# Kernel tuning notes

Hardware: AMD Instinct MI355X
Metric: run time of the kernel (lower is better)

The kernel has to match this reference:

```python
import jax, jax.numpy as jnp
import numpy as np

B, C, H, W = 4, 128, 96, 96
INTER = C // 2


def setup_inputs() -> dict:
    key = jax.random.key(0)
    ks = jax.random.split(key, 6)
    scale = 1.0 / np.sqrt(C)
    return {
        "x1": jax.random.normal(ks[0], (B, C, H, W), dtype=jnp.float32),
        "x2": jax.random.normal(ks[1], (B, C, H, W), dtype=jnp.float32),
        "w_theta": jax.random.normal(ks[2], (INTER, C), dtype=jnp.float32) * scale,
        "w_phi": jax.random.normal(ks[3], (INTER, C), dtype=jnp.float32) * scale,
        "w_g": jax.random.normal(ks[4], (INTER, C), dtype=jnp.float32) * scale,
        "w_mask": jax.random.normal(ks[5], (C, INTER), dtype=jnp.float32) * (1.0 / np.sqrt(INTER)),
    }


def reference(x1, x2, w_theta, w_phi, w_g, w_mask):
    b, c, h1, w1 = x1.shape  # c == full channel
    inter = c // 2
    # 1x1 convs (no bias) == channel GEMMs
    theta = jnp.einsum('ic,bchw->bihw', w_theta, x1)   # [b, inter, h1, w1]
    phi   = jnp.einsum('ic,bchw->bihw', w_phi,   x2)   # [b, inter, h2, w2]
    g     = jnp.einsum('ic,bchw->bihw', w_g,     x2)   # [b, inter, h2, w2]
    # Faithful to original: .view(b, c, -1) with c = FULL channel count,
    # so the flattened length is H*W/2 and the contraction dim is c (row-major reshape).
    theta = theta.reshape(b, c, -1).transpose(0, 2, 1)  # [b, N1, c], N1 = h1*w1//2
    phi = phi.reshape(b, c, -1)                         # [b, c, N2]
    g = g.reshape(b, c, -1).transpose(0, 2, 1)          # [b, N2, c]
    scores = jnp.einsum('bnc,bcm->bnm', theta, phi)     # [b, N1, N2]
    attn = jax.nn.softmax(scores, axis=1)               # softmax over dim=1 (query axis!)
    y = jnp.einsum('bnm,bmc->bnc', attn, g)             # [b, N1, c]
    y = y.transpose(0, 2, 1).reshape(b, inter, h1, w1)  # [b, inter, h1, w1]
    mask = jnp.einsum('ci,bihw->bchw', w_mask, y)       # [b, c, h1, w1]
    return mask + x1
```

## Files before the change

### kernel.cpp

```cpp
#include <hip/hip_runtime.h>

typedef __attribute__((ext_vector_type(8))) short short8;
typedef __attribute__((ext_vector_type(4))) float f32x4;
typedef __attribute__((ext_vector_type(16))) float f32x16;
typedef unsigned short u16;
typedef unsigned int u32;

#define NB 4
#define CH 128
#define INTER2 64
#define HW2 9216
#define NN 4608
#define NSLICE 8
#define SLW 576
#define SK 8
#define PCH 136

__device__ __forceinline__ u16 f2bf(float f) {
  u32 u = __float_as_uint(f);
  u += 0x7fffu + ((u >> 16) & 1u);
  return (u16)(u >> 16);
}
__device__ __forceinline__ float bf2f(u16 h) { return __uint_as_float(((u32)h) << 16); }
__device__ __forceinline__ u32 cvtpk(float lo, float hi) {
  u32 r;
  asm("v_cvt_pk_bf16_f32 %0, %1, %2" : "=v"(r) : "v"(lo), "v"(hi));
  return r;
}
__device__ __forceinline__ void gl_lds16(const u16* g, u16* l) {
  __builtin_amdgcn_global_load_lds(
      (const __attribute__((address_space(1))) unsigned int*)g,
      (__attribute__((address_space(3))) unsigned int*)l, 16, 0, 0);
}

__global__ void k_wcvt(const float* __restrict__ wt, const float* __restrict__ wp,
                       const float* __restrict__ wg, const float* __restrict__ wm,
                       u16* __restrict__ wtb, u16* __restrict__ wpb,
                       u16* __restrict__ wgb, u16* __restrict__ wmb) {
  int i = blockIdx.x * 256 + threadIdx.x;
  if (i < CH * INTER2) {
    wtb[i] = f2bf(wt[i]);
    wpb[i] = f2bf(wp[i]);
    wgb[i] = f2bf(wg[i]);
    wmb[i] = f2bf(wm[i]);
  }
}

__global__ __launch_bounds__(256) void k_conv(const float* __restrict__ x1,
                                              const float* __restrict__ x2,
                                              const u16* __restrict__ wtb,
                                              const u16* __restrict__ wpb,
                                              const u16* __restrict__ wgb,
                                              u16* __restrict__ Tt,
                                              u16* __restrict__ Pt,
                                              u16* __restrict__ Gn) {
  __shared__ u16 xT[64 * PCH];
  __shared__ u16 ot[64 * 72];
  const int tid = threadIdx.x;
  const int w = tid >> 6, l = tid & 63, lr = l & 15, lg = l >> 4;
  const int pt = blockIdx.x, b = blockIdx.y, z = blockIdx.z;
  const int p0 = pt * 64;
  const int h = (p0 >= NN) ? 1 : 0;
  const int n0 = p0 - h * NN;
  const float* X = (z ? x2 : x1) + (size_t)b * CH * HW2;

  {
    const int pq = (l & 15) * 4;
    const int cs = w + 4 * (l >> 4);
#pragma unroll
    for (int it = 0; it < 8; it++) {
      const int c = it * 16 + cs;
      float4 v = *(const float4*)(X + (size_t)c * HW2 + p0 + pq);
      xT[(pq + 0) * PCH + c] = f2bf(v.x);
      xT[(pq + 1) * PCH + c] = f2bf(v.y);
      xT[(pq + 2) * PCH + c] = f2bf(v.z);
      xT[(pq + 3) * PCH + c] = f2bf(v.w);
    }
  }
  short8 wsP[4], wsG[4];
  {
    const u16* W1 = z ? wpb : wtb;
#pragma unroll
    for (int ks = 0; ks < 4; ks++)
      wsP[ks] = *(const short8*)(W1 + (w * 16 + lr) * CH + ks * 32 + lg * 8);
    if (z) {
#pragma unroll
      for (int ks = 0; ks < 4; ks++)
        wsG[ks] = *(const short8*)(wgb + (w * 16 + lr) * CH + ks * 32 + lg * 8);
    }
  }
  __syncthreads();
  short8 xf[4][4];
#pragma unroll
  for (int tp = 0; tp < 4; tp++)
#pragma unroll
    for (int ks = 0; ks < 4; ks++)
      xf[tp][ks] = *(const short8*)(&xT[(tp * 16 + lr) * PCH + ks * 32 + lg * 8]);

  f32x4 accP[4];
#pragma unroll
  for (int tp = 0; tp < 4; tp++) {
#pragma unroll
    for (int j = 0; j < 4; j++) accP[tp][j] = 0.f;
#pragma unroll
    for (int ks = 0; ks < 4; ks++)
      accP[tp] = __builtin_amdgcn_mfma_f32_16x16x32_bf16(xf[tp][ks], wsP[ks], accP[tp], 0, 0, 0);
  }
#pragma unroll
  for (int tp = 0; tp < 4; tp++) {
#pragma unroll
    for (int j = 0; j < 4; j++)
      ot[(tp * 16 + lg * 4 + j) * 72 + w * 16 + lr] = f2bf(accP[tp][j]);
  }
  if (z) {
    f32x4 accG[4];
#pragma unroll
    for (int tp = 0; tp < 4; tp++) {
#pragma unroll
      for (int j = 0; j < 4; j++) accG[tp][j] = 0.f;
#pragma unroll
      for (int ks = 0; ks < 4; ks++)
        accG[tp] = __builtin_amdgcn_mfma_f32_16x16x32_bf16(wsG[ks], xf[tp][ks], accG[tp], 0, 0, 0);
    }
    u16* Gb = Gn + (size_t)b * CH * NN;
#pragma unroll
    for (int tp = 0; tp < 4; tp++) {
#pragma unroll
      for (int j = 0; j < 4; j++) {
        const int ig = w * 16 + lg * 4 + j;
        Gb[(size_t)((h << 6) + ig) * NN + n0 + tp * 16 + lr] = f2bf(accG[tp][j]);
      }
    }
  }
  __syncthreads();
  {
    u16* dst = (z ? Pt : Tt) + (size_t)b * NN * CH;
#pragma unroll
    for (int q = 0; q < 2; q++) {
      const int idx = tid * 2 + q;
      const int p = idx >> 3, c8 = (idx & 7) * 8;
      uint4 v = *(const uint4*)(&ot[p * 72 + c8]);
      *(uint4*)(dst + (size_t)(n0 + p) * CH + h * 64 + c8) = v;
    }
  }
}

__global__ __launch_bounds__(256) void k_scores(const u16* __restrict__ Tt,
                                                const u16* __restrict__ Pt,
                                                u16* __restrict__ E,
                                                float* __restrict__ denp,
                                                int b0) {
  __shared__ u16 Et[64 * 72];
  const int tid = threadIdx.x;
  const int w = tid >> 6, l = tid & 63, lm = l & 31, lh = l >> 5;
  const int wm2 = w >> 1, wn2 = w & 1;
  const int s = blockIdx.x & 7, mt = blockIdx.x >> 3;
  const int eb = blockIdx.y, b = b0 + eb;
  const int m0 = mt * 64;
  const int nbase = s * SLW;
  const u16* PtB = Pt + (size_t)b * NN * CH;
  const u16* TtB = Tt + (size_t)b * NN * CH;
  u16* Eb = E + (size_t)eb * NN * NN;

  short8 bf[8];
#pragma unroll
  for (int ks = 0; ks < 8; ks++)
    bf[ks] = *(const short8*)(PtB + (size_t)(m0 + wm2 * 32 + lm) * CH + ks * 16 + lh * 8);

  float den_l = 0.f;
  short8 ac[8], an[8];
#pragma unroll
  for (int ks = 0; ks < 8; ks++)
    ac[ks] = *(const short8*)(TtB + (size_t)(nbase + wn2 * 32 + lm) * CH + ks * 16 + lh * 8);

  for (int it = 0; it < 9; it++) {
    if (it + 1 < 9) {
      const int nr = nbase + (it + 1) * 64 + wn2 * 32 + lm;
#pragma unroll
      for (int ks = 0; ks < 8; ks++)
        an[ks] = *(const short8*)(TtB + (size_t)nr * CH + ks * 16 + lh * 8);
    }
    f32x16 acc;
#pragma unroll
    for (int q = 0; q < 16; q++) acc[q] = 0.f;
#pragma unroll
    for (int ks = 0; ks < 8; ks++)
      acc = __builtin_amdgcn_mfma_f32_32x32x16_bf16(ac[ks], bf[ks], acc, 0, 0, 0);
#pragma unroll
    for (int q = 0; q < 16; q += 2) {
      const int nl = wn2 * 32 + (q & 3) + 8 * (q >> 2) + 4 * lh;
      float e0 = exp2f(__builtin_fmaf(acc[q], 1.44269504f, -57.70780163f));
      float e1 = exp2f(__builtin_fmaf(acc[q + 1], 1.44269504f, -57.70780163f));
      den_l += e0;
      den_l += e1;
      u32 pk = cvtpk(e0, e1);
      Et[nl * 72 + wm2 * 32 + lm] = (u16)pk;
      Et[(nl + 1) * 72 + wm2 * 32 + lm] = (u16)(pk >> 16);
    }
    __syncthreads();
    {
      const int row0 = tid >> 3, col = (tid & 7) * 8;
      const int ng = nbase + it * 64;
#pragma unroll
      for (int p = 0; p < 2; p++) {
        const int r2 = p * 32 + row0;
        uint4 v = *(const uint4*)(&Et[r2 * 72 + col]);
        *(uint4*)(Eb + (size_t)(ng + r2) * NN + m0 + col) = v;
      }
    }
    __syncthreads();
    if (it + 1 < 9) {
#pragma unroll
      for (int ks = 0; ks < 8; ks++) ac[ks] = an[ks];
    }
  }
  den_l += __shfl_xor(den_l, 32, 64);
  __shared__ float dl[4][32];
  if (l < 32) dl[w][l] = den_l;
  __syncthreads();
  if (tid < 64)
    denp[(size_t)(s * NB + b) * NN + m0 + tid] =
        dl[(tid >> 5) * 2][tid & 31] + dl[(tid >> 5) * 2 + 1][tid & 31];
}

__global__ __launch_bounds__(256) void k_gd(const u16* __restrict__ Gn,
                                            const float* __restrict__ denp,
                                            u16* __restrict__ Gd,
                                            int b0) {
  const int q = blockIdx.x * 256 + threadIdx.x;
  const int d = q / 576, mc = q % 576;
  const int m0 = mc * 8;
  const int b = b0 + blockIdx.y;
  float dn[8];
#pragma unroll
  for (int i = 0; i < 8; i++) dn[i] = 0.f;
#pragma unroll
  for (int s = 0; s < NSLICE; s++) {
    const float* dp = denp + (size_t)(s * NB + b) * NN + m0;
    float4 a = *(const float4*)dp;
    float4 c = *(const float4*)(dp + 4);
    dn[0] += a.x; dn[1] += a.y; dn[2] += a.z; dn[3] += a.w;
    dn[4] += c.x; dn[5] += c.y; dn[6] += c.z; dn[7] += c.w;
  }
  const size_t off = (size_t)b * CH * NN + (size_t)d * NN + m0;
  uint4 v = *(const uint4*)(Gn + off);
  u32 arr[4] = {v.x, v.y, v.z, v.w};
  uint4 o;
  u32 ov[4];
#pragma unroll
  for (int j = 0; j < 4; j++) {
    float lo = bf2f((u16)(arr[j] & 0xffffu)) / dn[2 * j];
    float hi = bf2f((u16)(arr[j] >> 16)) / dn[2 * j + 1];
    ov[j] = cvtpk(lo, hi);
  }
  o.x = ov[0]; o.y = ov[1]; o.z = ov[2]; o.w = ov[3];
  *(uint4*)(Gd + off) = o;
}

__global__ __launch_bounds__(256) void k_pv(const u16* __restrict__ E,
                                            const u16* __restrict__ Gd,
                                            float* __restrict__ Yp,
                                            int b0) {
  __shared__ u16 lA[128 * 64];
  __shared__ u16 lB[128 * 64];
  const int tid = threadIdx.x;
  const int w = tid >> 6, l = tid & 63, lr = l & 15, lg = l >> 4;
  const int sk = blockIdx.x / 36, nt = blockIdx.x % 36;
  const int eb = blockIdx.y, b = b0 + eb;
  const int n0 = nt * 128;
  const int k0 = sk * (NN / SK);
  const u16* Eb = E + (size_t)eb * NN * NN;
  const u16* Gb = Gd + (size_t)b * CH * NN;
  const int wm = w >> 1, wn2 = w & 1;
  const int rl = l >> 3;
  const int cg = (l & 7) ^ rl;

  f32x4 acc[4][4];
#pragma unroll
  for (int fa = 0; fa < 4; fa++)
#pragma unroll
    for (int fb = 0; fb < 4; fb++)
#pragma unroll
      for (int j = 0; j < 4; j++) acc[fa][fb][j] = 0.f;

#define STAGE(kk)                                                                   \
  {                                                                                 \
    _Pragma("unroll") for (int r = 0; r < 4; r++) {                                 \
      const int rowA = r * 32 + w * 8 + rl;                                         \
      gl_lds16(Gb + (size_t)rowA * NN + (kk) + cg * 8, &lA[(r * 32 + w * 8) * 64]); \
      gl_lds16(Eb + (size_t)(n0 + rowA) * NN + (kk) + cg * 8,                       \
               &lB[(r * 32 + w * 8) * 64]);                                         \
    }                                                                               \
  }

  STAGE(k0);
  const int NKS = (NN / SK) / 64;
  for (int st = 0; st < NKS; st++) {
    __syncthreads();
#pragma unroll
    for (int ks2 = 0; ks2 < 2; ks2++) {
      const int cw = ((ks2 * 4 + lg) ^ (lr & 7)) * 8;
      short8 af[4], bfr[4];
#pragma unroll
      for (int fa = 0; fa < 4; fa++)
        af[fa] = *(const short8*)(&lA[(wm * 64 + fa * 16 + lr) * 64 + cw]);
#pragma unroll
      for (int fb = 0; fb < 4; fb++)
        bfr[fb] = *(const short8*)(&lB[(wn2 * 64 + fb * 16 + lr) * 64 + cw]);
#pragma unroll
      for (int fa = 0; fa < 4; fa++)
#pragma unroll
        for (int fb = 0; fb < 4; fb++)
          acc[fa][fb] = __builtin_amdgcn_mfma_f32_16x16x32_bf16(af[fa], bfr[fb], acc[fa][fb], 0, 0, 0);
    }
    __syncthreads();
    if (st + 1 < NKS) STAGE(k0 + (st + 1) * 64);
  }
#undef STAGE
  const int slab = sk * 2 + eb;
  float* Yb = Yp + (size_t)slab * CH * NN;
#pragma unroll
  for (int fa = 0; fa < 4; fa++) {
#pragma unroll
    for (int fb = 0; fb < 4; fb++) {
      const int n = n0 + wn2 * 64 + fb * 16 + lr;
#pragma unroll
      for (int j = 0; j < 4; j++) {
        const int cc = wm * 64 + fa * 16 + lg * 4 + j;
        Yb[(size_t)cc * NN + n] = acc[fa][fb][j];
      }
    }
  }
}

__global__ __launch_bounds__(256) void k_out(const float* __restrict__ Yp,
                                             const u16* __restrict__ wmb,
                                             const float* __restrict__ x1,
                                             float* __restrict__ out,
                                             int b0) {
  __shared__ u16 yy[64][72];
  const int tid = threadIdx.x;
  const int w = tid >> 6, l = tid & 63, lr = l & 15, lg = l >> 4;
  const int eb = blockIdx.y, b = b0 + eb;
  const int n0 = blockIdx.x * 32;
  const int nl = tid & 31, cch = tid >> 5;

  float v[16];
#pragma unroll
  for (int q = 0; q < 16; q++) v[q] = 0.f;
  for (int s2 = 0; s2 < SK; s2++) {
    const float* base = Yp + ((size_t)(s2 * 2 + eb) * CH + cch * 16) * NN + n0 + nl;
#pragma unroll
    for (int q = 0; q < 16; q++) v[q] += base[(size_t)q * NN];
  }
#pragma unroll
  for (int q = 0; q < 16; q++) {
    const int d = cch * 16 + q;
    yy[(d >> 6) * 32 + nl][d & 63] = f2bf(v[q]);
  }
  __syncthreads();

  const int wm3 = w >> 1, wp3 = w & 1;
  f32x4 eacc[4][2];
#pragma unroll
  for (int fa = 0; fa < 4; fa++)
#pragma unroll
    for (int fb = 0; fb < 2; fb++)
#pragma unroll
      for (int j = 0; j < 4; j++) eacc[fa][fb][j] = 0.f;
#pragma unroll
  for (int ks = 0; ks < 2; ks++) {
    short8 wa[4];
#pragma unroll
    for (int fa = 0; fa < 4; fa++)
      wa[fa] = *(const short8*)(wmb + (wm3 * 64 + fa * 16 + lr) * 64 + ks * 32 + lg * 8);
    short8 yb[2];
#pragma unroll
    for (int fb = 0; fb < 2; fb++)
      yb[fb] = *(const short8*)(&yy[wp3 * 32 + fb * 16 + lr][ks * 32 + lg * 8]);
#pragma unroll
    for (int fa = 0; fa < 4; fa++)
#pragma unroll
      for (int fb = 0; fb < 2; fb++)
        eacc[fa][fb] = __builtin_amdgcn_mfma_f32_16x16x32_bf16(wa[fa], yb[fb], eacc[fa][fb], 0, 0, 0);
  }
  const float* x1b = x1 + (size_t)b * CH * HW2;
  float* ob = out + (size_t)b * CH * HW2;
#pragma unroll
  for (int fa = 0; fa < 4; fa++) {
#pragma unroll
    for (int fb = 0; fb < 2; fb++) {
      const int pl = wp3 * 32 + fb * 16 + lr;
      const int col = n0 + (pl & 31) + (pl >> 5) * NN;
#pragma unroll
      for (int j = 0; j < 4; j++) {
        const int c = wm3 * 64 + fa * 16 + lg * 4 + j;
        const size_t o = (size_t)c * HW2 + col;
        ob[o] = eacc[fa][fb][j] + x1b[o];
      }
    }
  }
}

extern "C" void kernel_launch(void* const* d_in, const int* in_sizes, int n_in,
                              void* d_out, int out_size, void* d_ws, size_t ws_size,
                              hipStream_t stream) {
  const float* x1 = (const float*)d_in[0];
  const float* x2 = (const float*)d_in[1];
  const float* wt = (const float*)d_in[2];
  const float* wp = (const float*)d_in[3];
  const float* wg = (const float*)d_in[4];
  const float* wm = (const float*)d_in[5];
  float* out = (float*)d_out;

  char* ws = (char*)d_ws;
  const size_t SZ_T = (size_t)NB * NN * CH * 2;
  u16* Tt = (u16*)ws; ws += SZ_T;
  u16* Pt = (u16*)ws; ws += SZ_T;
  u16* Gn = (u16*)ws; ws += SZ_T;
  u16* Gd = (u16*)ws; ws += SZ_T;
  float* denp = (float*)ws; ws += (size_t)NSLICE * NB * NN * 4;
  u16* wtb = (u16*)ws; ws += (size_t)CH * INTER2 * 2;
  u16* wpb = (u16*)ws; ws += (size_t)CH * INTER2 * 2;
  u16* wgb = (u16*)ws; ws += (size_t)CH * INTER2 * 2;
  u16* wmb = (u16*)ws; ws += (size_t)CH * INTER2 * 2;
  float* Yp = (float*)ws; ws += (size_t)16 * CH * NN * 4;
  u16* E = (u16*)ws;

  const size_t fixed = (size_t)(ws - (char*)d_ws);
  const size_t eslab = (size_t)NN * NN * 2;
  int eslots = 0;
  if (ws_size >= fixed + 2 * eslab) eslots = 2;
  else if (ws_size >= fixed + 1 * eslab) eslots = 1;
  if (eslots == 0) return;

  hipLaunchKernelGGL(k_wcvt, dim3(32), dim3(256), 0, stream, wt, wp, wg, wm, wtb, wpb, wgb, wmb);
  hipLaunchKernelGGL(k_conv, dim3(144, NB, 2), dim3(256), 0, stream, x1, x2, wtb, wpb, wgb, Tt, Pt, Gn);
  for (int b0 = 0; b0 < NB; b0 += eslots) {
    hipLaunchKernelGGL(k_scores, dim3(72 * 8, eslots), dim3(256), 0, stream, Tt, Pt, E, denp, b0);
    hipLaunchKernelGGL(k_gd, dim3(288, eslots), dim3(256), 0, stream, Gn, denp, Gd, b0);
    hipLaunchKernelGGL(k_pv, dim3(SK * 36, eslots), dim3(256), 0, stream, E, Gd, Yp, b0);
    hipLaunchKernelGGL(k_out, dim3(144, eslots), dim3(256), 0, stream, Yp, wmb, x1, out, b0);
  }
}
```

Measured before the change: 204.5 us.

## Fuse scores, PV and output projection into flash-style kernel, drop E matrix

Replaces the materialized NxN exp-score matrix and split-K PV reduction with a denominator-only pass followed by a fused kernel. The fused kernel recomputes scores per 32-row query tile, exponentiates into LDS, multiplies by the normalized G, and applies the output projection plus residual directly. This removes the large E writes/reads and the Yp partial buffers and batches all images in single launches, at the cost of computing the score GEMM twice and having only 576 blocks each looping over 36 chunks serially.

New measurement: 305.5 us. +49.4%, slower.

```diff
diff --git a/kernel.cpp b/kernel.cpp
--- a/kernel.cpp
+++ b/kernel.cpp
@@ -13,7 +13,6 @@
 #define NN 4608
 #define NSLICE 8
 #define SLW 576
-#define SK 8
 #define PCH 136
 
 __device__ __forceinline__ u16 f2bf(float f) {
@@ -145,22 +144,18 @@
   }
 }
 
-__global__ __launch_bounds__(256) void k_scores(const u16* __restrict__ Tt,
-                                                const u16* __restrict__ Pt,
-                                                u16* __restrict__ E,
-                                                float* __restrict__ denp,
-                                                int b0) {
-  __shared__ u16 Et[64 * 72];
+__global__ __launch_bounds__(256) void k_den(const u16* __restrict__ Tt,
+                                             const u16* __restrict__ Pt,
+                                             float* __restrict__ denp) {
   const int tid = threadIdx.x;
   const int w = tid >> 6, l = tid & 63, lm = l & 31, lh = l >> 5;
   const int wm2 = w >> 1, wn2 = w & 1;
   const int s = blockIdx.x & 7, mt = blockIdx.x >> 3;
-  const int eb = blockIdx.y, b = b0 + eb;
+  const int b = blockIdx.y;
   const int m0 = mt * 64;
   const int nbase = s * SLW;
   const u16* PtB = Pt + (size_t)b * NN * CH;
   const u16* TtB = Tt + (size_t)b * NN * CH;
-  u16* Eb = E + (size_t)eb * NN * NN;
 
   short8 bf[8];
 #pragma unroll
@@ -187,28 +182,8 @@
     for (int ks = 0; ks < 8; ks++)
       acc = __builtin_amdgcn_mfma_f32_32x32x16_bf16(ac[ks], bf[ks], acc, 0, 0, 0);
 #pragma unroll
-    for (int q = 0; q < 16; q += 2) {
-      const int nl = wn2 * 32 + (q & 3) + 8 * (q >> 2) + 4 * lh;
-      float e0 = exp2f(__builtin_fmaf(acc[q], 1.44269504f, -57.70780163f));
-      float e1 = exp2f(__builtin_fmaf(acc[q + 1], 1.44269504f, -57.70780163f));
-      den_l += e0;
-      den_l += e1;
-      u32 pk = cvtpk(e0, e1);
-      Et[nl * 72 + wm2 * 32 + lm] = (u16)pk;
-      Et[(nl + 1) * 72 + wm2 * 32 + lm] = (u16)(pk >> 16);
-    }
-    __syncthreads();
-    {
-      const int row0 = tid >> 3, col = (tid & 7) * 8;
-      const int ng = nbase + it * 64;
-#pragma unroll
-      for (int p = 0; p < 2; p++) {
-        const int r2 = p * 32 + row0;
-        uint4 v = *(const uint4*)(&Et[r2 * 72 + col]);
-        *(uint4*)(Eb + (size_t)(ng + r2) * NN + m0 + col) = v;
-      }
-    }
-    __syncthreads();
+    for (int q = 0; q < 16; q++)
+      den_l += exp2f(__builtin_fmaf(acc[q], 1.44269504f, -57.70780163f));
     if (it + 1 < 9) {
 #pragma unroll
       for (int ks = 0; ks < 8; ks++) ac[ks] = an[ks];
@@ -225,12 +200,11 @@
 
 __global__ __launch_bounds__(256) void k_gd(const u16* __restrict__ Gn,
                                             const float* __restrict__ denp,
-                                            u16* __restrict__ Gd,
-                                            int b0) {
+                                            u16* __restrict__ Gd) {
   const int q = blockIdx.x * 256 + threadIdx.x;
   const int d = q / 576, mc = q % 576;
   const int m0 = mc * 8;
-  const int b = b0 + blockIdx.y;
+  const int b = blockIdx.y;
   float dn[8];
 #pragma unroll
   for (int i = 0; i < 8; i++) dn[i] = 0.f;
@@ -257,109 +231,123 @@
   *(uint4*)(Gd + off) = o;
 }
 
-__global__ __launch_bounds__(256) void k_pv(const u16* __restrict__ E,
-                                            const u16* __restrict__ Gd,
-                                            float* __restrict__ Yp,
-                                            int b0) {
-  __shared__ u16 lA[128 * 64];
-  __shared__ u16 lB[128 * 64];
-  const int tid = threadIdx.x;
-  const int w = tid >> 6, l = tid & 63, lr = l & 15, lg = l >> 4;
-  const int sk = blockIdx.x / 36, nt = blockIdx.x % 36;
-  const int eb = blockIdx.y, b = b0 + eb;
-  const int n0 = nt * 128;
-  const int k0 = sk * (NN / SK);
-  const u16* Eb = E + (size_t)eb * NN * NN;
-  const u16* Gb = Gd + (size_t)b * CH * NN;
-  const int wm = w >> 1, wn2 = w & 1;
-  const int rl = l >> 3;
-  const int cg = (l & 7) ^ rl;
-
-  f32x4 acc[4][4];
-#pragma unroll
-  for (int fa = 0; fa < 4; fa++)
-#pragma unroll
-    for (int fb = 0; fb < 4; fb++)
-#pragma unroll
-      for (int j = 0; j < 4; j++) acc[fa][fb][j] = 0.f;
-
-#define STAGE(kk)                                                                   \
-  {                                                                                 \
-    _Pragma("unroll") for (int r = 0; r < 4; r++) {                                 \
-      const int rowA = r * 32 + w * 8 + rl;                                         \
-      gl_lds16(Gb + (size_t)rowA * NN + (kk) + cg * 8, &lA[(r * 32 + w * 8) * 64]); \
-      gl_lds16(Eb + (size_t)(n0 + rowA) * NN + (kk) + cg * 8,                       \
-               &lB[(r * 32 + w * 8) * 64]);                                         \
-    }                                                                               \
-  }
-
-  STAGE(k0);
-  const int NKS = (NN / SK) / 64;
-  for (int st = 0; st < NKS; st++) {
-    __syncthreads();
-#pragma unroll
-    for (int ks2 = 0; ks2 < 2; ks2++) {
-      const int cw = ((ks2 * 4 + lg) ^ (lr & 7)) * 8;
-      short8 af[4], bfr[4];
-#pragma unroll
-      for (int fa = 0; fa < 4; fa++)
-        af[fa] = *(const short8*)(&lA[(wm * 64 + fa * 16 + lr) * 64 + cw]);
-#pragma unroll
-      for (int fb = 0; fb < 4; fb++)
-        bfr[fb] = *(const short8*)(&lB[(wn2 * 64 + fb * 16 + lr) * 64 + cw]);
-#pragma unroll
-      for (int fa = 0; fa < 4; fa++)
-#pragma unroll
-        for (int fb = 0; fb < 4; fb++)
-          acc[fa][fb] = __builtin_amdgcn_mfma_f32_16x16x32_bf16(af[fa], bfr[fb], acc[fa][fb], 0, 0, 0);
-    }
-    __syncthreads();
-    if (st + 1 < NKS) STAGE(k0 + (st + 1) * 64);
-  }
-#undef STAGE
-  const int slab = sk * 2 + eb;
-  float* Yb = Yp + (size_t)slab * CH * NN;
-#pragma unroll
-  for (int fa = 0; fa < 4; fa++) {
-#pragma unroll
-    for (int fb = 0; fb < 4; fb++) {
-      const int n = n0 + wn2 * 64 + fb * 16 + lr;
-#pragma unroll
-      for (int j = 0; j < 4; j++) {
-        const int cc = wm * 64 + fa * 16 + lg * 4 + j;
-        Yb[(size_t)cc * NN + n] = acc[fa][fb][j];
-      }
-    }
-  }
-}
-
-__global__ __launch_bounds__(256) void k_out(const float* __restrict__ Yp,
-                                             const u16* __restrict__ wmb,
-                                             const float* __restrict__ x1,
-                                             float* __restrict__ out,
-                                             int b0) {
+__global__ __launch_bounds__(256) void k_fused(const u16* __restrict__ Tt,
+                                               const u16* __restrict__ Pt,
+                                               const u16* __restrict__ Gd,
+                                               const u16* __restrict__ wmb,
+                                               const float* __restrict__ x1,
+                                               float* __restrict__ out) {
+  __shared__ u16 TtS[32 * 128];
+  __shared__ u16 Atile[32][136];
   __shared__ u16 yy[64][72];
   const int tid = threadIdx.x;
   const int w = tid >> 6, l = tid & 63, lr = l & 15, lg = l >> 4;
-  const int eb = blockIdx.y, b = b0 + eb;
-  const int n0 = blockIdx.x * 32;
-  const int nl = tid & 31, cch = tid >> 5;
-
-  float v[16];
-#pragma unroll
-  for (int q = 0; q < 16; q++) v[q] = 0.f;
-  for (int s2 = 0; s2 < SK; s2++) {
-    const float* base = Yp + ((size_t)(s2 * 2 + eb) * CH + cch * 16) * NN + n0 + nl;
-#pragma unroll
-    for (int q = 0; q < 16; q++) v[q] += base[(size_t)q * NN];
-  }
-#pragma unroll
-  for (int q = 0; q < 16; q++) {
-    const int d = cch * 16 + q;
-    yy[(d >> 6) * 32 + nl][d & 63] = f2bf(v[q]);
+  const int lm = l & 31, lh = l >> 5;
+  const int gid = blockIdx.x;
+  const int xcd = gid & 7;
+  const int b = xcd >> 1;
+  const int nt = (gid >> 3) * 2 + (xcd & 1);
+  const int n0 = nt * 32;
+  const u16* TtB = Tt + ((size_t)b * NN + n0) * CH;
+  const u16* PtB = Pt + (size_t)b * NN * CH;
+  const u16* GdB = Gd + (size_t)b * CH * NN;
+
+#pragma unroll
+  for (int it = 0; it < 2; it++) {
+    const int i = it * 256 + w * 64 + l;
+    const int row = i >> 4, slot = i & 15;
+    gl_lds16(TtB + (size_t)row * CH + (slot ^ (row & 15)) * 8,
+             &TtS[(it * 256 + w * 64) * 8]);
   }
   __syncthreads();
 
+  short8 af[8];
+#pragma unroll
+  for (int ks = 0; ks < 8; ks++)
+    af[ks] = *(const short8*)(&TtS[lm * 128 + (((ks * 2 + lh) ^ (lm & 15)) * 8)]);
+
+  f32x4 acc[2][2];
+#pragma unroll
+  for (int fc = 0; fc < 2; fc++)
+#pragma unroll
+    for (int fn = 0; fn < 2; fn++)
+#pragma unroll
+      for (int j = 0; j < 4; j++) acc[fc][fn][j] = 0.f;
+
+  short8 pf[8], pfn[8], gf[2][4], gfn[2][4];
+#pragma unroll
+  for (int ks = 0; ks < 8; ks++)
+    pf[ks] = *(const short8*)(PtB + (size_t)(w * 32 + lm) * CH + ks * 16 + lh * 8);
+#pragma unroll
+  for (int fc = 0; fc < 2; fc++)
+#pragma unroll
+    for (int ks = 0; ks < 4; ks++)
+      gf[fc][ks] = *(const short8*)(GdB + (size_t)(w * 32 + fc * 16 + lr) * NN + ks * 32 + lg * 8);
+
+  for (int ch = 0; ch < 36; ch++) {
+    const int mch = ch * 128;
+    if (ch + 1 < 36) {
+      const int mn = mch + 128;
+#pragma unroll
+      for (int ks = 0; ks < 8; ks++)
+        pfn[ks] = *(const short8*)(PtB + (size_t)(mn + w * 32 + lm) * CH + ks * 16 + lh * 8);
+    }
+    f32x16 sacc;
+#pragma unroll
+    for (int q = 0; q < 16; q++) sacc[q] = 0.f;
+#pragma unroll
+    for (int ks = 0; ks < 8; ks++)
+      sacc = __builtin_amdgcn_mfma_f32_32x32x16_bf16(af[ks], pf[ks], sacc, 0, 0, 0);
+#pragma unroll
+    for (int q = 0; q < 16; q++) {
+      const int nl = (q & 3) + 8 * (q >> 2) + 4 * lh;
+      float e = exp2f(__builtin_fmaf(sacc[q], 1.44269504f, -57.70780163f));
+      Atile[nl][w * 32 + lm] = f2bf(e);
+    }
+    __syncthreads();
+    if (ch + 1 < 36) {
+      const int mn = mch + 128;
+#pragma unroll
+      for (int fc = 0; fc < 2; fc++)
+#pragma unroll
+        for (int ks = 0; ks < 4; ks++)
+          gfn[fc][ks] = *(const short8*)(GdB + (size_t)(w * 32 + fc * 16 + lr) * NN + mn + ks * 32 + lg * 8);
+    }
+#pragma unroll
+    for (int ks = 0; ks < 4; ks++) {
+      short8 ab[2];
+#pragma unroll
+      for (int fn = 0; fn < 2; fn++)
+        ab[fn] = *(const short8*)(&Atile[fn * 16 + lr][ks * 32 + lg * 8]);
+#pragma unroll
+      for (int fc = 0; fc < 2; fc++)
+#pragma unroll
+        for (int fn = 0; fn < 2; fn++)
+          acc[fc][fn] = __builtin_amdgcn_mfma_f32_16x16x32_bf16(gf[fc][ks], ab[fn], acc[fc][fn], 0, 0, 0);
+    }
+    __syncthreads();
+    if (ch + 1 < 36) {
+#pragma unroll
+      for (int ks = 0; ks < 8; ks++) pf[ks] = pfn[ks];
+#pragma unroll
+      for (int fc = 0; fc < 2; fc++)
+#pragma unroll
+        for (int ks = 0; ks < 4; ks++) gf[fc][ks] = gfn[fc][ks];
+    }
+  }
+#pragma unroll
+  for (int fc = 0; fc < 2; fc++) {
+#pragma unroll
+    for (int fn = 0; fn < 2; fn++) {
+      const int nl = fn * 16 + lr;
+#pragma unroll
+      for (int j = 0; j < 4; j++) {
+        const int c = w * 32 + fc * 16 + lg * 4 + j;
+        yy[(c >> 6) * 32 + nl][c & 63] = f2bf(acc[fc][fn][j]);
+      }
+    }
+  }
+  __syncthreads();
   const int wm3 = w >> 1, wp3 = w & 1;
   f32x4 eacc[4][2];
 #pragma unroll
@@ -424,22 +412,11 @@
   u16* wpb = (u16*)ws; ws += (size_t)CH * INTER2 * 2;
   u16* wgb = (u16*)ws; ws += (size_t)CH * INTER2 * 2;
   u16* wmb = (u16*)ws; ws += (size_t)CH * INTER2 * 2;
-  float* Yp = (float*)ws; ws += (size_t)16 * CH * NN * 4;
-  u16* E = (u16*)ws;
-
-  const size_t fixed = (size_t)(ws - (char*)d_ws);
-  const size_t eslab = (size_t)NN * NN * 2;
-  int eslots = 0;
-  if (ws_size >= fixed + 2 * eslab) eslots = 2;
-  else if (ws_size >= fixed + 1 * eslab) eslots = 1;
-  if (eslots == 0) return;
+  if (ws_size < (size_t)(ws - (char*)d_ws)) return;
 
   hipLaunchKernelGGL(k_wcvt, dim3(32), dim3(256), 0, stream, wt, wp, wg, wm, wtb, wpb, wgb, wmb);
   hipLaunchKernelGGL(k_conv, dim3(144, NB, 2), dim3(256), 0, stream, x1, x2, wtb, wpb, wgb, Tt, Pt, Gn);
-  for (int b0 = 0; b0 < NB; b0 += eslots) {
-    hipLaunchKernelGGL(k_scores, dim3(72 * 8, eslots), dim3(256), 0, stream, Tt, Pt, E, denp, b0);
-    hipLaunchKernelGGL(k_gd, dim3(288, eslots), dim3(256), 0, stream, Gn, denp, Gd, b0);
-    hipLaunchKernelGGL(k_pv, dim3(SK * 36, eslots), dim3(256), 0, stream, E, Gd, Yp, b0);
-    hipLaunchKernelGGL(k_out, dim3(144, eslots), dim3(256), 0, stream, Yp, wmb, x1, out, b0);
-  }
-}
+  hipLaunchKernelGGL(k_den, dim3(576, NB), dim3(256), 0, stream, Tt, Pt, denp);
+  hipLaunchKernelGGL(k_gd, dim3(288, NB), dim3(256), 0, stream, Gn, denp, Gd);
+  hipLaunchKernelGGL(k_fused, dim3(576), dim3(256), 0, stream, Tt, Pt, Gd, wmb, x1, out);
+}
```

## Reshape score tiles to 32x256 per block with 16 N-slices

Applied to the files above, without the earlier changes.

Each k_scores block now covers 256 key columns and 32 query rows per iteration. Each wave holds two 32-column B fragments and issues two MFMAs per A fragment, and the grid doubles the N slices to 16. The change aims to write longer contiguous rows of the exp-score matrix E, and to reuse each loaded Tt fragment across more MFMAs. In exchange the kernel launches fewer blocks, holds more registers for the second B fragment, and uses scalar f2bf rounding in place of the packed convert instruction. k_gd now sums 16 partial denominators per column instead of 8.

Result: slower. 208.7 us (+2.1%).

```diff
diff --git a/kernel.cpp b/kernel.cpp
--- a/kernel.cpp
+++ b/kernel.cpp
@@ -11,10 +11,11 @@
 #define INTER2 64
 #define HW2 9216
 #define NN 4608
-#define NSLICE 8
-#define SLW 576
+#define NSLICE 16
+#define SLW2 288
 #define SK 8
 #define PCH 136
+#define EPITCH 264
 
 __device__ __forceinline__ u16 f2bf(float f) {
   u32 u = __float_as_uint(f);
@@ -150,62 +151,64 @@
                                                 u16* __restrict__ E,
                                                 float* __restrict__ denp,
                                                 int b0) {
-  __shared__ u16 Et[64 * 72];
+  __shared__ u16 Et[32 * EPITCH];
   const int tid = threadIdx.x;
   const int w = tid >> 6, l = tid & 63, lm = l & 31, lh = l >> 5;
-  const int wm2 = w >> 1, wn2 = w & 1;
-  const int s = blockIdx.x & 7, mt = blockIdx.x >> 3;
+  const int s = blockIdx.x & 15, mt = blockIdx.x >> 4;
   const int eb = blockIdx.y, b = b0 + eb;
-  const int m0 = mt * 64;
-  const int nbase = s * SLW;
+  const int m0 = mt * 256;
+  const int nbase = s * SLW2;
   const u16* PtB = Pt + (size_t)b * NN * CH;
   const u16* TtB = Tt + (size_t)b * NN * CH;
   u16* Eb = E + (size_t)eb * NN * NN;
 
-  short8 bf[8];
+  short8 bf[2][8];
+#pragma unroll
+  for (int ms = 0; ms < 2; ms++)
+#pragma unroll
+    for (int ks = 0; ks < 8; ks++)
+      bf[ms][ks] = *(const short8*)(PtB + (size_t)(m0 + w * 64 + ms * 32 + lm) * CH + ks * 16 + lh * 8);
+
+  float den0 = 0.f, den1 = 0.f;
+  short8 ac[8], an[8];
 #pragma unroll
   for (int ks = 0; ks < 8; ks++)
-    bf[ks] = *(const short8*)(PtB + (size_t)(m0 + wm2 * 32 + lm) * CH + ks * 16 + lh * 8);
-
-  float den_l = 0.f;
-  short8 ac[8], an[8];
-#pragma unroll
-  for (int ks = 0; ks < 8; ks++)
-    ac[ks] = *(const short8*)(TtB + (size_t)(nbase + wn2 * 32 + lm) * CH + ks * 16 + lh * 8);
+    ac[ks] = *(const short8*)(TtB + (size_t)(nbase + lm) * CH + ks * 16 + lh * 8);
 
   for (int it = 0; it < 9; it++) {
     if (it + 1 < 9) {
-      const int nr = nbase + (it + 1) * 64 + wn2 * 32 + lm;
+      const int nr = nbase + (it + 1) * 32 + lm;
 #pragma unroll
       for (int ks = 0; ks < 8; ks++)
         an[ks] = *(const short8*)(TtB + (size_t)nr * CH + ks * 16 + lh * 8);
     }
-    f32x16 acc;
-#pragma unroll
-    for (int q = 0; q < 16; q++) acc[q] = 0.f;
-#pragma unroll
-    for (int ks = 0; ks < 8; ks++)
-      acc = __builtin_amdgcn_mfma_f32_32x32x16_bf16(ac[ks], bf[ks], acc, 0, 0, 0);
-#pragma unroll
-    for (int q = 0; q < 16; q += 2) {
-      const int nl = wn2 * 32 + (q & 3) + 8 * (q >> 2) + 4 * lh;
-      float e0 = exp2f(__builtin_fmaf(acc[q], 1.44269504f, -57.70780163f));
-      float e1 = exp2f(__builtin_fmaf(acc[q + 1], 1.44269504f, -57.70780163f));
-      den_l += e0;
-      den_l += e1;
-      u32 pk = cvtpk(e0, e1);
-      Et[nl * 72 + wm2 * 32 + lm] = (u16)pk;
-      Et[(nl + 1) * 72 + wm2 * 32 + lm] = (u16)(pk >> 16);
+    f32x16 a0, a1;
+#pragma unroll
+    for (int q = 0; q < 16; q++) { a0[q] = 0.f; a1[q] = 0.f; }
+#pragma unroll
+    for (int ks = 0; ks < 8; ks++) {
+      a0 = __builtin_amdgcn_mfma_f32_32x32x16_bf16(ac[ks], bf[0][ks], a0, 0, 0, 0);
+      a1 = __builtin_amdgcn_mfma_f32_32x32x16_bf16(ac[ks], bf[1][ks], a1, 0, 0, 0);
+    }
+#pragma unroll
+    for (int q = 0; q < 16; q++) {
+      const int nl = (q & 3) + 8 * (q >> 2) + 4 * lh;
+      float e0 = exp2f(__builtin_fmaf(a0[q], 1.44269504f, -57.70780163f));
+      float e1 = exp2f(__builtin_fmaf(a1[q], 1.44269504f, -57.70780163f));
+      den0 += e0;
+      den1 += e1;
+      Et[nl * EPITCH + w * 64 + lm] = f2bf(e0);
+      Et[nl * EPITCH + w * 64 + 32 + lm] = f2bf(e1);
     }
     __syncthreads();
     {
-      const int row0 = tid >> 3, col = (tid & 7) * 8;
-      const int ng = nbase + it * 64;
-#pragma unroll
-      for (int p = 0; p < 2; p++) {
-        const int r2 = p * 32 + row0;
-        uint4 v = *(const uint4*)(&Et[r2 * 72 + col]);
-        *(uint4*)(Eb + (size_t)(ng + r2) * NN + m0 + col) = v;
+      const int r = tid >> 3, cq = tid & 7;
+      const int ng = nbase + it * 32 + r;
+      u16* dst = Eb + (size_t)ng * NN + m0;
+#pragma unroll
+      for (int k = 0; k < 4; k++) {
+        const int col = k * 64 + cq * 8;
+        *(uint4*)(dst + col) = *(const uint4*)(&Et[r * EPITCH + col]);
       }
     }
     __syncthreads();
@@ -214,13 +217,13 @@
       for (int ks = 0; ks < 8; ks++) ac[ks] = an[ks];
     }
   }
-  den_l += __shfl_xor(den_l, 32, 64);
-  __shared__ float dl[4][32];
-  if (l < 32) dl[w][l] = den_l;
-  __syncthreads();
-  if (tid < 64)
-    denp[(size_t)(s * NB + b) * NN + m0 + tid] =
-        dl[(tid >> 5) * 2][tid & 31] + dl[(tid >> 5) * 2 + 1][tid & 31];
+  den0 += __shfl_xor(den0, 32, 64);
+  den1 += __shfl_xor(den1, 32, 64);
+  if (l < 32) {
+    float* dp = denp + (size_t)(s * NB + b) * NN + m0 + w * 64;
+    dp[lm] = den0;
+    dp[32 + lm] = den1;
+  }
 }
 
 __global__ __launch_bounds__(256) void k_gd(const u16* __restrict__ Gn,
@@ -437,7 +440,7 @@
   hipLaunchKernelGGL(k_wcvt, dim3(32), dim3(256), 0, stream, wt, wp, wg, wm, wtb, wpb, wgb, wmb);
   hipLaunchKernelGGL(k_conv, dim3(144, NB, 2), dim3(256), 0, stream, x1, x2, wtb, wpb, wgb, Tt, Pt, Gn);
   for (int b0 = 0; b0 < NB; b0 += eslots) {
-    hipLaunchKernelGGL(k_scores, dim3(72 * 8, eslots), dim3(256), 0, stream, Tt, Pt, E, denp, b0);
+    hipLaunchKernelGGL(k_scores, dim3(18 * 16, eslots), dim3(256), 0, stream, Tt, Pt, E, denp, b0);
     hipLaunchKernelGGL(k_gd, dim3(288, eslots), dim3(256), 0, stream, Gn, denp, Gd, b0);
     hipLaunchKernelGGL(k_pv, dim3(SK * 36, eslots), dim3(256), 0, stream, E, Gd, Yp, b0);
     hipLaunchKernelGGL(k_out, dim3(144, eslots), dim3(256), 0, stream, Yp, wmb, x1, out, b0);
```
